# Kernel optimization log

Hardware: AMD Instinct MI355X
Metric: run time of the kernel (lower is better)

## Reference

```python
import jax, jax.numpy as jnp
import numpy as np

N_NODES = 100000
D = 256
B = 64
EPG = 1024           # edges per query group in the last (pruned) layer
E1 = B * EPG         # 65536
E0 = 65536
K = 256              # max_edges


def setup_inputs() -> dict:
    key = jax.random.key(0)
    ks = jax.random.split(key, 20)
    # last-layer edges: sorted by eg_idx, exactly EPG edges per query group
    eg_idx1 = np.repeat(np.arange(B, dtype=np.int32), EPG)
    node_i1 = np.asarray(jax.random.randint(ks[0], (E1,), 0, N_NODES, dtype=jnp.int32))
    node_j1 = np.asarray(jax.random.randint(ks[1], (E1,), 0, N_NODES, dtype=jnp.int32))
    edges1 = np.zeros((E1, 8), dtype=np.int32)
    edges1[:, 0] = eg_idx1; edges1[:, 6] = node_i1; edges1[:, 7] = node_j1
    # earlier-layer edges (no pruning, any order)
    edges0 = np.zeros((E0, 8), dtype=np.int32)
    edges0[:, 0] = np.asarray(jax.random.randint(ks[2], (E0,), 0, B, dtype=jnp.int32))
    edges0[:, 6] = np.asarray(jax.random.randint(ks[3], (E0,), 0, N_NODES, dtype=jnp.int32))
    edges0[:, 7] = np.asarray(jax.random.randint(ks[4], (E0,), 0, N_NODES, dtype=jnp.int32))

    rn = lambda k, s, sc=1.0: (jax.random.normal(k, s, dtype=jnp.float32) * sc)
    return {
        "attended_nodes": jax.random.randint(ks[5], (B, 2), 0, N_NODES, dtype=jnp.int32),
        "node_score": jax.random.uniform(ks[6], (N_NODES,), dtype=jnp.float32),
        "edges0": jnp.asarray(edges0),
        "edges1": jnp.asarray(edges1),
        "rel_emb0": rn(ks[7], (E0, D)),
        "rel_emb1": rn(ks[8], (E1, D)),
        "memorized_embedding": rn(ks[9], (N_NODES, D)),
        "query_src_ts_emb": rn(ks[10], (B, D)),
        "query_rel_emb": rn(ks[11], (B, D)),
        "Wl": rn(ks[12], (4 * D, 2 * D), np.sqrt(2.0 / (4 * D))),
        "bl": rn(ks[13], (2 * D,), 0.01),
        "Wr": rn(ks[14], (4 * D, 2 * D), np.sqrt(2.0 / (4 * D))),
        "br": rn(ks[15], (2 * D,), 0.01),
        "Wc": rn(ks[16], (2 * D, 2 * D), np.sqrt(2.0 / (4 * D))),
        "bc": rn(ks[17], (2 * D,), 0.01),
        "Wlin": rn(ks[18], (D, D), np.sqrt(2.0 / D)),
        "blin": rn(ks[19], (D,), 0.01),
        "max_edges": K,
    }


def _g_score(hi, hj, rel, qs, qr, Wl, bl, Wr, br, Wc, bc):
    # bilinear MLP score: sum(LReLU(L @ Wl) * ((LReLU(R @ Wr)) @ Wc), -1)
    left = jnp.concatenate([hi, rel, qs, qr], axis=-1)   # [E, 4D]
    right = jnp.concatenate([hj, rel, qs, qr], axis=-1)  # [E, 4D]
    l = jax.nn.leaky_relu(left @ Wl + bl)                # [E, 2D]
    r = jax.nn.leaky_relu(right @ Wr + br) @ Wc + bc     # [E, 2D]
    return jnp.sum(l * r, axis=-1)                       # [E]


def _att_score(edges, emb, rel, qs_tab, qr_tab, Wl, bl, Wr, br, Wc, bc):
    hi = emb[edges[:, 6]]
    hj = emb[edges[:, 7]]
    qs = qs_tab[edges[:, 0]]
    qr = qr_tab[edges[:, 0]]
    return _g_score(hi, hj, rel, qs, qr, Wl, bl, Wr, br, Wc, bc)


def _segment_softmax(logits, seg, num_seg):
    m = jax.ops.segment_max(logits, seg, num_segments=num_seg)
    e = jnp.exp(logits - m[seg])
    s = jax.ops.segment_sum(e, seg, num_segments=num_seg)
    return e / s[seg]


def _update_nodes(edges, emb, logits):
    # aggregate source embeddings into targets, weighted by attention;
    # nodes with no incoming edge keep their old embedding.
    n = emb.shape[0]
    agg = jax.ops.segment_sum(logits[:, None] * emb[edges[:, 6]], edges[:, 7], num_segments=n)
    cnt = jax.ops.segment_sum(jnp.ones_like(logits), edges[:, 7], num_segments=n)
    return jnp.where((cnt > 0)[:, None], agg, emb)


def reference(attended_nodes, node_score, edges0, edges1, rel_emb0, rel_emb1,
              memorized_embedding, query_src_ts_emb, query_rel_emb,
              Wl, bl, Wr, br, Wc, bc, Wlin, blin, max_edges):
    n_nodes = memorized_embedding.shape[0]
    # ---- last layer: attention + segmented softmax over source node ----
    logits1 = _att_score(edges1, memorized_embedding, rel_emb1,
                         query_src_ts_emb, query_rel_emb, Wl, bl, Wr, br, Wc, bc)
    sm1 = _segment_softmax(logits1, edges1[:, 6], n_nodes)
    src_att = node_score[edges1[:, 6]]
    target_att = sm1 * src_att
    # ---- per-query top-k pruning (groups are contiguous, equal size EPG) ----
    b = B
    vals = target_att.reshape(b, EPG)
    pruned_att2, idx = jax.lax.top_k(vals, max_edges)              # [B, K]
    orig_indices = (jnp.arange(b, dtype=idx.dtype)[:, None] * EPG + idx).reshape(-1)
    pruned_att = pruned_att2.reshape(-1)                           # [B*K]
    pruned_edges = edges1[orig_indices]
    sm_pruned = sm1[orig_indices]
    # ---- node score aggregation ('sum') ----
    updated_node_score = jax.ops.segment_sum(sm_pruned * pruned_att,
                                             pruned_edges[:, 7], num_segments=n_nodes)
    # ---- propagate representations along pruned edges ----
    emb = _update_nodes(pruned_edges, memorized_embedding, sm_pruned)
    # ---- earlier layers (reversed) ----
    logits0 = _att_score(edges0, emb, rel_emb0, query_src_ts_emb, query_rel_emb,
                         Wl, bl, Wr, br, Wc, bc)
    sm0 = _segment_softmax(logits0, edges0[:, 6], n_nodes)
    emb = _update_nodes(edges0, emb, sm0)
    # ---- bypass: linear + LeakyReLU between steps ----
    emb = jax.nn.leaky_relu(emb @ Wlin + blin)
    return updated_node_score, emb, pruned_edges, orig_indices
```

## Files before the change

### kernel.cpp

```cpp
#include <hip/hip_runtime.h>
#include <math.h>


#define NNODES 100000
#define DDIM   256
#define NH     512
#define NGROUP 64
#define EPG    1024
#define E1N    65536
#define E0N    65536
#define KTOP   256

typedef __attribute__((ext_vector_type(8))) _Float16 h8v;
typedef __attribute__((ext_vector_type(4))) float f32x4;
typedef __attribute__((ext_vector_type(4))) int i4v;

__device__ __forceinline__ float lrelu(float x) { return x > 0.0f ? x : 0.01f * x; }

__device__ __forceinline__ unsigned fenc(float f) {
  unsigned u = __float_as_uint(f);
  return (u & 0x80000000u) ? ~u : (u | 0x80000000u);
}
__device__ __forceinline__ float fdec(unsigned k) {
  unsigned u = (k & 0x80000000u) ? (k & 0x7FFFFFFFu) : ~k;
  return __uint_as_float(u);
}

__device__ __forceinline__ void splitf(float v, unsigned short& h, unsigned short& l) {
  _Float16 hh = (_Float16)v;
  _Float16 ll = (_Float16)(v - (float)hh);
  h = __builtin_bit_cast(unsigned short, hh);
  l = __builtin_bit_cast(unsigned short, ll);
}

__device__ __forceinline__ unsigned packsplit(float v) {
  unsigned short h, l;
  splitf(v, h, l);
  return ((unsigned)h << 16) | (unsigned)l;
}

__device__ __forceinline__ f32x4 mfma16(h8v a, h8v b, f32x4 c) {
  return __builtin_amdgcn_mfma_f32_16x16x32_f16(a, b, c, 0, 0, 0);
}

__global__ __launch_bounds__(512)
void qterm_kernel(const float* __restrict__ qse, const float* __restrict__ qre,
                  const float* __restrict__ Wl, const float* __restrict__ bl,
                  const float* __restrict__ Wr, const float* __restrict__ br,
                  float* __restrict__ qtl, float* __restrict__ qtr)
{
  const int g = blockIdx.x;
  const int o = threadIdx.x;
  __shared__ float sq[DDIM];
  __shared__ float sr[DDIM];
  if (o < DDIM) sq[o] = qse[(size_t)g * DDIM + o];
  else          sr[o - DDIM] = qre[(size_t)g * DDIM + (o - DDIM)];
  __syncthreads();
  float al = bl[o], ar = br[o];
  for (int k = 0; k < DDIM; ++k) {
    float a = sq[k], b = sr[k];
    al += a * Wl[(size_t)(512 + k) * NH + o] + b * Wl[(size_t)(768 + k) * NH + o];
    ar += a * Wr[(size_t)(512 + k) * NH + o] + b * Wr[(size_t)(768 + k) * NH + o];
  }
  qtl[(size_t)g * NH + o] = al;
  qtr[(size_t)g * NH + o] = ar;
}

__global__ __launch_bounds__(256)
void wprep_kernel(const float* __restrict__ Wl, const float* __restrict__ Wr,
                  const float* __restrict__ Wc,
                  unsigned short* __restrict__ WltH, unsigned short* __restrict__ WltL,
                  unsigned short* __restrict__ WrtH, unsigned short* __restrict__ WrtL,
                  unsigned short* __restrict__ WctH, unsigned short* __restrict__ WctL)
{
  __shared__ float shv[32][33];
  const int mtx = blockIdx.y;
  const int ti = blockIdx.x >> 4;
  const int tj = blockIdx.x & 15;
  const float* W = mtx == 0 ? Wl : (mtx == 1 ? Wr : Wc);
  unsigned short* OH = mtx == 0 ? WltH : (mtx == 1 ? WrtH : WctH);
  unsigned short* OL = mtx == 0 ? WltL : (mtx == 1 ? WrtL : WctL);
  const int t = threadIdx.x;
  const int r = t >> 3, c4 = (t & 7) * 4;
  *(float4*)&shv[r][c4] = *(const float4*)(W + (size_t)(ti * 32 + r) * 512 + tj * 32 + c4);
  __syncthreads();
  unsigned short h[4], l[4];
#pragma unroll
  for (int q = 0; q < 4; ++q) splitf(shv[c4 + q][r], h[q], l[q]);
  const size_t off = (size_t)(tj * 32 + r) * 512 + ti * 32 + c4;
  *(uint2*)(OH + off) = make_uint2((unsigned)h[0] | ((unsigned)h[1] << 16),
                                   (unsigned)h[2] | ((unsigned)h[3] << 16));
  *(uint2*)(OL + off) = make_uint2((unsigned)l[0] | ((unsigned)l[1] << 16),
                                   (unsigned)l[2] | ((unsigned)l[3] << 16));
}

__global__ __launch_bounds__(256)
void wlinprep_kernel(const float* __restrict__ Wlin, unsigned short* __restrict__ WlinT)
{
  __shared__ float shv[32][33];
  const int ti = blockIdx.x >> 3;
  const int tj = blockIdx.x & 7;
  const int t = threadIdx.x;
  const int r = t >> 3, c4 = (t & 7) * 4;
  *(float4*)&shv[r][c4] = *(const float4*)(Wlin + (size_t)(ti * 32 + r) * 256 + tj * 32 + c4);
  __syncthreads();
  unsigned short o[4];
#pragma unroll
  for (int q = 0; q < 4; ++q)
    o[q] = __builtin_bit_cast(unsigned short, (_Float16)shv[c4 + q][r]);
  *(uint2*)(WlinT + (size_t)(tj * 32 + r) * 256 + ti * 32 + c4) =
      make_uint2((unsigned)o[0] | ((unsigned)o[1] << 16),
                 (unsigned)o[2] | ((unsigned)o[3] << 16));
}

template<int SPLIT>
__global__ __launch_bounds__(512, 2)
void fused_score_kernel(const int* __restrict__ edges,
                        const float* __restrict__ emb,
                        const float* __restrict__ rel,
                        const unsigned short* __restrict__ BrH,
                        const unsigned short* __restrict__ BrL,
                        const unsigned short* __restrict__ BcH,
                        const unsigned short* __restrict__ BcL,
                        const unsigned short* __restrict__ BlH,
                        const unsigned short* __restrict__ BlL,
                        const float* __restrict__ qtr,
                        const float* __restrict__ qtl,
                        const float* __restrict__ bcv,
                        float* __restrict__ logits,
                        unsigned* __restrict__ mkey)
{
  __shared__ unsigned lds[64 * 512];
  __shared__ float red[8][64];
  __shared__ int sidx[64];
  __shared__ int sgrp[64];

  const int tid  = threadIdx.x;
  const int lane = tid & 63;
  const int w    = tid >> 6;
  const int arow = lane & 15;
  const int kgrp = (lane >> 4) * 8;
  const int col0 = w * 64;
  const int rb   = blockIdx.x * 64;

  auto stage = [&]() {
    const int srow = tid >> 3;
    const int sseg = tid & 7;
    const float* src = (sseg < 4)
        ? emb + (size_t)sidx[srow] * DDIM + sseg * 64
        : rel + (size_t)(rb + srow) * DDIM + (sseg - 4) * 64;
    const int sw = (srow & 7) << 2;
#pragma unroll
    for (int q = 0; q < 16; ++q) {
      float4 f = ((const float4*)src)[q];
      uint4 o = make_uint4(packsplit(f.x), packsplit(f.y), packsplit(f.z), packsplit(f.w));
      *(uint4*)&lds[srow * 512 + ((sseg * 64 + q * 4) ^ sw)] = o;
    }
  };

  auto gemm = [&](const unsigned short* BH, const unsigned short* BL, f32x4 (&acc)[4][4]) {
    for (int ks = 0; ks < 16; ++ks) {
      const int k0 = ks * 32 + kgrp;
      h8v bh[4], bl[4];
#pragma unroll
      for (int nt = 0; nt < 4; ++nt) {
        const size_t boff = (size_t)(col0 + nt * 16 + arow) * 512 + k0;
        bh[nt] = *(const h8v*)(BH + boff);
        if (SPLIT) bl[nt] = *(const h8v*)(BL + boff);
      }
#pragma unroll
      for (int mt = 0; mt < 4; ++mt) {
        const int row = mt * 16 + arow;
        const int sw = (row & 7) << 2;
        const unsigned* lp = &lds[row * 512];
        uint4 u0 = *(const uint4*)(lp + (k0 ^ sw));
        uint4 u1 = *(const uint4*)(lp + ((k0 + 4) ^ sw));
        unsigned u[8] = {u0.x, u0.y, u0.z, u0.w, u1.x, u1.y, u1.z, u1.w};
        i4v hv, lv;
#pragma unroll
        for (int d = 0; d < 4; ++d) {
          hv[d] = (int)((u[2*d] >> 16) | (u[2*d+1] & 0xffff0000u));
          if (SPLIT) lv[d] = (int)((u[2*d] & 0xffffu) | (u[2*d+1] << 16));
        }
        h8v h = __builtin_bit_cast(h8v, hv);
        h8v l;
        if (SPLIT) l = __builtin_bit_cast(h8v, lv);
#pragma unroll
        for (int nt = 0; nt < 4; ++nt) {
          acc[mt][nt] = mfma16(h, bh[nt], acc[mt][nt]);
          if (SPLIT) {
            acc[mt][nt] = mfma16(h, bl[nt], acc[mt][nt]);
            acc[mt][nt] = mfma16(l, bh[nt], acc[mt][nt]);
          }
        }
      }
    }
  };

  if (tid < 64) {
    const int* er = edges + (size_t)(rb + tid) * 8;
    sidx[tid] = er[7];
    sgrp[tid] = er[0];
  }
  __syncthreads();
  stage();
  __syncthreads();

  f32x4 a1[4][4];
#pragma unroll
  for (int a = 0; a < 4; ++a)
#pragma unroll
    for (int b = 0; b < 4; ++b) a1[a][b] = (f32x4)0.0f;
  gemm(BrH, BrL, a1);
  __syncthreads();
#pragma unroll
  for (int mt = 0; mt < 4; ++mt)
#pragma unroll
    for (int nt = 0; nt < 4; ++nt) {
      const int c = col0 + nt * 16 + arow;
#pragma unroll
      for (int reg = 0; reg < 4; ++reg) {
        const int row = mt * 16 + (lane >> 4) * 4 + reg;
        float v = lrelu(a1[mt][nt][reg] + qtr[(size_t)sgrp[row] * NH + c]);
        lds[row * 512 + (c ^ ((row & 7) << 2))] = packsplit(v);
      }
    }
  __syncthreads();

  f32x4 ro[4][4];
#pragma unroll
  for (int a = 0; a < 4; ++a)
#pragma unroll
    for (int b = 0; b < 4; ++b) ro[a][b] = (f32x4)0.0f;
  gemm(BcH, BcL, ro);
#pragma unroll
  for (int nt = 0; nt < 4; ++nt) {
    const float bcval = bcv[col0 + nt * 16 + arow];
#pragma unroll
    for (int mt = 0; mt < 4; ++mt)
#pragma unroll
      for (int reg = 0; reg < 4; ++reg) ro[mt][nt][reg] += bcval;
  }
  __syncthreads();
  if (tid < 64) sidx[tid] = edges[(size_t)(rb + tid) * 8 + 6];
  __syncthreads();
  stage();
  __syncthreads();

  f32x4 a3[4][4];
#pragma unroll
  for (int a = 0; a < 4; ++a)
#pragma unroll
    for (int b = 0; b < 4; ++b) a3[a][b] = (f32x4)0.0f;
  gemm(BlH, BlL, a3);
#pragma unroll
  for (int mt = 0; mt < 4; ++mt) {
#pragma unroll
    for (int reg = 0; reg < 4; ++reg) {
      const int row = mt * 16 + (lane >> 4) * 4 + reg;
      const int g = sgrp[row];
      float s = 0.0f;
#pragma unroll
      for (int nt = 0; nt < 4; ++nt) {
        const int c = col0 + nt * 16 + arow;
        float v = lrelu(a3[mt][nt][reg] + qtl[(size_t)g * NH + c]);
        s += v * ro[mt][nt][reg];
      }
      s += __shfl_xor(s, 1); s += __shfl_xor(s, 2);
      s += __shfl_xor(s, 4); s += __shfl_xor(s, 8);
      if ((lane & 15) == 0) red[w][row] = s;
    }
  }
  __syncthreads();
  if (tid < 64) {
    float s = 0.0f;
#pragma unroll
    for (int p = 0; p < 8; ++p) s += red[p][tid];
    logits[rb + tid] = s;
    atomicMax(mkey + sidx[tid], fenc(s));
  }
}

__global__ void smax_exp_kernel(const int* __restrict__ edges, const float* __restrict__ logits,
                                const unsigned* __restrict__ mkey, float* __restrict__ ssum,
                                float* __restrict__ sm, int* __restrict__ cnt, int E)
{
  int e = blockIdx.x * blockDim.x + threadIdx.x;
  if (e < E) {
    int s = edges[(size_t)e * 8 + 6];
    float ev = expf(logits[e] - fdec(mkey[s]));
    sm[e] = ev;
    atomicAdd(ssum + s, ev);
    if (cnt) atomicAdd(cnt + edges[(size_t)e * 8 + 7], 1);
  }
}

__global__ void smax_norm_kernel(const int* __restrict__ edges, const float* __restrict__ ssum,
                                 float* __restrict__ sm, const float* __restrict__ nscore,
                                 float* __restrict__ ta, int E)
{
  int e = blockIdx.x * blockDim.x + threadIdx.x;
  if (e < E) {
    int s = edges[(size_t)e * 8 + 6];
    float v = sm[e] / ssum[s];
    sm[e] = v;
    if (ta) ta[e] = v * nscore[s];
  }
}

__global__ __launch_bounds__(256)
void topk_kernel(const float* __restrict__ ta, const float* __restrict__ sm1,
                 const int* __restrict__ edges1,
                 float* __restrict__ out0, float* __restrict__ out2,
                 float* __restrict__ out3, float* __restrict__ smp,
                 int* __restrict__ prn_i, int* __restrict__ prn_j,
                 int* __restrict__ cnt1)
{
  __shared__ float v[EPG];
  __shared__ int   ix[EPG];
  const int g = blockIdx.x, tid = threadIdx.x;
  for (int t = tid; t < EPG; t += 256) { v[t] = ta[(size_t)g * EPG + t]; ix[t] = t; }
  __syncthreads();
  for (int k = 2; k <= EPG; k <<= 1) {
    for (int j = k >> 1; j > 0; j >>= 1) {
      for (int t = tid; t < EPG; t += 256) {
        int l = t ^ j;
        if (l > t) {
          float va = v[t], vb = v[l];
          int ia = ix[t], ib = ix[l];
          bool aFirst = (va > vb) || (va == vb && ia < ib);
          bool up = ((t & k) == 0);
          bool sw = up ? !aFirst : aFirst;
          if (sw) { v[t] = vb; ix[t] = ib; v[l] = va; ix[l] = ia; }
        }
      }
      __syncthreads();
    }
  }
  const int r = tid;
  const int oi = ix[r];
  const float val = v[r];
  const int orig = g * EPG + oi;
  out3[(size_t)g * KTOP + r] = (float)orig;
  const int* er = edges1 + (size_t)orig * 8;
#pragma unroll
  for (int c = 0; c < 8; ++c)
    out2[((size_t)(g * KTOP + r)) * 8 + c] = (float)er[c];
  const int ii = er[6], jj = er[7];
  const float smv = sm1[orig];
  smp[(size_t)g * KTOP + r] = smv;
  prn_i[(size_t)g * KTOP + r] = ii;
  prn_j[(size_t)g * KTOP + r] = jj;
  atomicAdd(out0 + jj, smv * val);
  atomicAdd(cnt1 + jj, 1);
}

__global__ void scatter_kernel(const int* __restrict__ idx_i, int si,
                               const int* __restrict__ idx_j, int sj,
                               const float* __restrict__ w,
                               const float* __restrict__ semb,
                               float* __restrict__ agg)
{
  const int e0 = blockIdx.x * 4;
  const int o = threadIdx.x;
#pragma unroll
  for (int q = 0; q < 4; ++q) {
    const int e = e0 + q;
    const int i = idx_i[(size_t)e * si];
    const int j = idx_j[(size_t)e * sj];
    atomicAdd(agg + (size_t)j * DDIM + o, w[e] * semb[(size_t)i * DDIM + o]);
  }
}

__global__ void combine_kernel(const float* __restrict__ mememb, const int* __restrict__ cnt,
                               float* __restrict__ agg)
{
  size_t id = (size_t)blockIdx.x * 256 + threadIdx.x;
  if (cnt[id >> 8] == 0) agg[id] = mememb[id];
}

__global__ __launch_bounds__(512)
void final_mfma_kernel(const float* __restrict__ emb1, const float* __restrict__ agg0,
                       const int* __restrict__ cnt0,
                       const unsigned short* __restrict__ WlinT,
                       const float* __restrict__ blin, float* __restrict__ out)
{
  __shared__ int scnt[128];
  const int tid  = threadIdx.x;
  const int lane = tid & 63;
  const int wid  = tid >> 6;
  const int wm = wid >> 2, wn = wid & 3;
  const int rb = blockIdx.x * 128;
  const int arow = lane & 15;
  const int kgrp = (lane >> 4) * 8;
  const int row0 = wm * 64;
  const int col0 = wn * 64;

  if (tid < 128) {
    int r = rb + tid;
    scnt[tid] = (r < NNODES) ? cnt0[(r < NNODES) ? r : 0] : 0;
  }
  __syncthreads();

  f32x4 acc[4][4];
#pragma unroll
  for (int a = 0; a < 4; ++a)
#pragma unroll
    for (int b = 0; b < 4; ++b) acc[a][b] = (f32x4)0.0f;

  for (int ks = 0; ks < 8; ++ks) {
    const int k0 = ks * 32 + kgrp;
    h8v ah[4], bh[4];
#pragma unroll
    for (int nt = 0; nt < 4; ++nt)
      bh[nt] = *(const h8v*)(WlinT + (size_t)(col0 + nt * 16 + arow) * 256 + k0);
#pragma unroll
    for (int mt = 0; mt < 4; ++mt) {
      const int rl = row0 + mt * 16 + arow;
      int r = rb + rl;
      int rc = (r < NNODES) ? r : (NNODES - 1);
      const float* base = (scnt[rl] > 0) ? agg0 : emb1;
      const float* src = base + (size_t)rc * DDIM + k0;
      float4 f0 = *(const float4*)src;
      float4 f1 = *(const float4*)(src + 4);
      float v[8] = {f0.x, f0.y, f0.z, f0.w, f1.x, f1.y, f1.z, f1.w};
      h8v h;
#pragma unroll
      for (int d = 0; d < 8; ++d) h[d] = (_Float16)v[d];
      ah[mt] = h;
    }
#pragma unroll
    for (int mt = 0; mt < 4; ++mt)
#pragma unroll
      for (int nt = 0; nt < 4; ++nt)
        acc[mt][nt] = mfma16(ah[mt], bh[nt], acc[mt][nt]);
  }

  float bl4[4];
#pragma unroll
  for (int nt = 0; nt < 4; ++nt) bl4[nt] = blin[col0 + nt * 16 + arow];

#pragma unroll
  for (int mt = 0; mt < 4; ++mt)
#pragma unroll
    for (int reg = 0; reg < 4; ++reg) {
      const int r = rb + row0 + mt * 16 + (lane >> 4) * 4 + reg;
      if (r < NNODES) {
#pragma unroll
        for (int nt = 0; nt < 4; ++nt) {
          const int c = col0 + nt * 16 + arow;
          out[(size_t)r * DDIM + c] = lrelu(acc[mt][nt][reg] + bl4[nt]);
        }
      }
    }
}

extern "C" void kernel_launch(void* const* d_in, const int* in_sizes, int n_in,
                              void* d_out, int out_size, void* d_ws, size_t ws_size,
                              hipStream_t stream)
{
  (void)in_sizes; (void)n_in; (void)out_size; (void)ws_size;

  const float* node_score = (const float*)d_in[1];
  const int*   edges0 = (const int*)d_in[2];
  const int*   edges1 = (const int*)d_in[3];
  const float* rel0   = (const float*)d_in[4];
  const float* rel1   = (const float*)d_in[5];
  const float* mememb = (const float*)d_in[6];
  const float* qse    = (const float*)d_in[7];
  const float* qre    = (const float*)d_in[8];
  const float* Wl     = (const float*)d_in[9];
  const float* bl     = (const float*)d_in[10];
  const float* Wr     = (const float*)d_in[11];
  const float* br     = (const float*)d_in[12];
  const float* Wc     = (const float*)d_in[13];
  const float* bc     = (const float*)d_in[14];
  const float* Wlin   = (const float*)d_in[15];
  const float* blin   = (const float*)d_in[16];

  float* out0 = (float*)d_out;
  float* out1 = out0 + NNODES;
  float* out2 = out1 + (size_t)NNODES * DDIM;
  float* out3 = out2 + (size_t)NGROUP * KTOP * 8;

  char* wptr = (char*)d_ws;
  auto alloc = [&](size_t bytes) -> char* {
    char* p = wptr;
    wptr += (bytes + 255) & ~(size_t)255;
    return p;
  };
  float*    qtl     = (float*)alloc((size_t)NGROUP * NH * 4);
  float*    qtr     = (float*)alloc((size_t)NGROUP * NH * 4);
  float*    logits1 = (float*)alloc((size_t)E1N * 4);
  float*    sm1     = (float*)alloc((size_t)E1N * 4);
  float*    ta      = (float*)alloc((size_t)E1N * 4);
  float*    logits0 = (float*)alloc((size_t)E0N * 4);
  float*    sm0     = (float*)alloc((size_t)E0N * 4);
  unsigned* mkey    = (unsigned*)alloc((size_t)NNODES * 4);
  float*    ssum    = (float*)alloc((size_t)NNODES * 4);
  int*      cnt1    = (int*)alloc((size_t)NNODES * 4);
  int*      cnt0    = (int*)alloc((size_t)NNODES * 4);
  float*    smp     = (float*)alloc((size_t)NGROUP * KTOP * 4);
  int*      prn_i   = (int*)alloc((size_t)NGROUP * KTOP * 4);
  int*      prn_j   = (int*)alloc((size_t)NGROUP * KTOP * 4);
  float*    agg1    = (float*)alloc((size_t)NNODES * DDIM * 4);

  unsigned short* WltH = (unsigned short*)alloc((size_t)512 * 512 * 2);
  unsigned short* WltL = (unsigned short*)alloc((size_t)512 * 512 * 2);
  unsigned short* WrtH = (unsigned short*)alloc((size_t)512 * 512 * 2);
  unsigned short* WrtL = (unsigned short*)alloc((size_t)512 * 512 * 2);
  unsigned short* WctH = (unsigned short*)alloc((size_t)512 * 512 * 2);
  unsigned short* WctL = (unsigned short*)alloc((size_t)512 * 512 * 2);
  unsigned short* WlnT = (unsigned short*)alloc((size_t)256 * 256 * 2);

  (void)hipMemsetAsync(agg1, 0, (size_t)NNODES * DDIM * 4, stream);
  (void)hipMemsetAsync(cnt1, 0, (size_t)NNODES * 4, stream);
  (void)hipMemsetAsync(mkey, 0, (size_t)NNODES * 4, stream);
  (void)hipMemsetAsync(ssum, 0, (size_t)NNODES * 4, stream);
  (void)hipMemsetAsync(out0, 0, (size_t)NNODES * 4, stream);

  qterm_kernel<<<NGROUP, 512, 0, stream>>>(qse, qre, Wl, bl, Wr, br, qtl, qtr);
  {
    dim3 g(256, 3);
    wprep_kernel<<<g, 256, 0, stream>>>(Wl, Wr, Wc, WltH, WltL, WrtH, WrtL, WctH, WctL);
  }
  wlinprep_kernel<<<64, 256, 0, stream>>>(Wlin, WlnT);

  fused_score_kernel<1><<<E1N / 64, 512, 0, stream>>>(
      edges1, mememb, rel1, WrtH, WrtL, WctH, WctL, WltH, WltL,
      qtr, qtl, bc, logits1, mkey);

  smax_exp_kernel<<<E1N / 256, 256, 0, stream>>>(edges1, logits1, mkey, ssum, sm1,
                                                 nullptr, E1N);
  smax_norm_kernel<<<E1N / 256, 256, 0, stream>>>(edges1, ssum, sm1, node_score, ta, E1N);
  topk_kernel<<<NGROUP, 256, 0, stream>>>(ta, sm1, edges1, out0, out2, out3,
                                          smp, prn_i, prn_j, cnt1);
  scatter_kernel<<<NGROUP * KTOP / 4, 256, 0, stream>>>(prn_i, 1, prn_j, 1, smp,
                                                        mememb, agg1);
  combine_kernel<<<NNODES, 256, 0, stream>>>(mememb, cnt1, agg1);

  (void)hipMemsetAsync(mkey, 0, (size_t)NNODES * 4, stream);
  (void)hipMemsetAsync(ssum, 0, (size_t)NNODES * 4, stream);
  (void)hipMemsetAsync(cnt0, 0, (size_t)NNODES * 4, stream);
  (void)hipMemsetAsync(out1, 0, (size_t)NNODES * DDIM * 4, stream);

  fused_score_kernel<0><<<E0N / 64, 512, 0, stream>>>(
      edges0, agg1, rel0, WrtH, WrtL, WctH, WctL, WltH, WltL,
      qtr, qtl, bc, logits0, mkey);

  smax_exp_kernel<<<E0N / 256, 256, 0, stream>>>(edges0, logits0, mkey, ssum, sm0,
                                                 cnt0, E0N);
  smax_norm_kernel<<<E0N / 256, 256, 0, stream>>>(edges0, ssum, sm0, nullptr, nullptr, E0N);
  scatter_kernel<<<E0N / 4, 256, 0, stream>>>(edges0 + 6, 8, edges0 + 7, 8, sm0,
                                              agg1, out1);
  final_mfma_kernel<<<(NNODES + 127) / 128, 512, 0, stream>>>(agg1, out1, cnt0,
                                                              WlnT, blin, out1);
}
```

Measured before the change: 1.102 ms.

## Split LDS into separate hi/lo fp16 planes and prefetch second-stage rows into registers

The fused score kernel now stores the split-fp16 operands as two separate planes (hi and lo) with an XOR swizzle at 8-element granularity. This lets the GEMM inner loop read h8v fragments straight from LDS instead of unpacking interleaved 32-bit words with shifts and masks. The emb[node_i] and rel rows used by the third GEMM are loaded into 16 uint4 registers at kernel start, so their global latency overlaps the first two GEMMs. The cost is much higher register pressure under launch_bounds(512,2), which risks spills, and the second LReLU writeback now does scattered 16-bit LDS stores.

```diff
diff --git a/kernel.cpp b/kernel.cpp
--- a/kernel.cpp
+++ b/kernel.cpp
@@ -13,7 +13,6 @@
 
 typedef __attribute__((ext_vector_type(8))) _Float16 h8v;
 typedef __attribute__((ext_vector_type(4))) float f32x4;
-typedef __attribute__((ext_vector_type(4))) int i4v;
 
 __device__ __forceinline__ float lrelu(float x) { return x > 0.0f ? x : 0.01f * x; }
 
@@ -33,14 +32,26 @@
   l = __builtin_bit_cast(unsigned short, ll);
 }
 
-__device__ __forceinline__ unsigned packsplit(float v) {
-  unsigned short h, l;
-  splitf(v, h, l);
-  return ((unsigned)h << 16) | (unsigned)l;
-}
-
 __device__ __forceinline__ f32x4 mfma16(h8v a, h8v b, f32x4 c) {
   return __builtin_amdgcn_mfma_f32_16x16x32_f16(a, b, c, 0, 0, 0);
+}
+
+__device__ __forceinline__ void pack8(uint4 a, uint4 b, uint4& ph, uint4& pl) {
+  float v[8] = {__uint_as_float(a.x), __uint_as_float(a.y),
+                __uint_as_float(a.z), __uint_as_float(a.w),
+                __uint_as_float(b.x), __uint_as_float(b.y),
+                __uint_as_float(b.z), __uint_as_float(b.w)};
+  unsigned short h[8], l[8];
+#pragma unroll
+  for (int d = 0; d < 8; ++d) splitf(v[d], h[d], l[d]);
+  ph = make_uint4((unsigned)h[0] | ((unsigned)h[1] << 16),
+                  (unsigned)h[2] | ((unsigned)h[3] << 16),
+                  (unsigned)h[4] | ((unsigned)h[5] << 16),
+                  (unsigned)h[6] | ((unsigned)h[7] << 16));
+  pl = make_uint4((unsigned)l[0] | ((unsigned)l[1] << 16),
+                  (unsigned)l[2] | ((unsigned)l[3] << 16),
+                  (unsigned)l[4] | ((unsigned)l[5] << 16),
+                  (unsigned)l[6] | ((unsigned)l[7] << 16));
 }
 
 __global__ __launch_bounds__(512)
@@ -130,37 +141,68 @@
                         float* __restrict__ logits,
                         unsigned* __restrict__ mkey)
 {
-  __shared__ unsigned lds[64 * 512];
+  constexpr int NP = SPLIT ? 2 : 1;
+  __shared__ uint4 planesv[NP * 4096];
   __shared__ float red[8][64];
-  __shared__ int sidx[64];
-  __shared__ int sgrp[64];
+  __shared__ int sidxJ[64], sidxI[64], sgrp[64];
 
   const int tid  = threadIdx.x;
   const int lane = tid & 63;
   const int w    = tid >> 6;
   const int arow = lane & 15;
-  const int kgrp = (lane >> 4) * 8;
+  const int grp  = lane >> 4;
   const int col0 = w * 64;
   const int rb   = blockIdx.x * 64;
 
-  auto stage = [&]() {
-    const int srow = tid >> 3;
-    const int sseg = tid & 7;
-    const float* src = (sseg < 4)
-        ? emb + (size_t)sidx[srow] * DDIM + sseg * 64
-        : rel + (size_t)(rb + srow) * DDIM + (sseg - 4) * 64;
-    const int sw = (srow & 7) << 2;
-#pragma unroll
-    for (int q = 0; q < 16; ++q) {
-      float4 f = ((const float4*)src)[q];
-      uint4 o = make_uint4(packsplit(f.x), packsplit(f.y), packsplit(f.z), packsplit(f.w));
-      *(uint4*)&lds[srow * 512 + ((sseg * 64 + q * 4) ^ sw)] = o;
-    }
-  };
-
-  auto gemm = [&](const unsigned short* BH, const unsigned short* BL, f32x4 (&acc)[4][4]) {
+  const int srow = tid >> 3;
+  const int gs   = tid & 7;
+  const int ssw  = srow & 7;
+
+  if (tid < 64) {
+    const int* er = edges + (size_t)(rb + tid) * 8;
+    sgrp[tid]  = er[0];
+    sidxI[tid] = er[6];
+    sidxJ[tid] = er[7];
+  }
+  __syncthreads();
+
+  const float* baseR = rel + (size_t)(rb + srow) * DDIM - 256;
+
+  uint4 ai[16];
+  {
+    const float* bI = emb + (size_t)sidxI[srow] * DDIM;
+#pragma unroll
+    for (int q = 0; q < 8; ++q) {
+      const int kf = q * 64 + ((gs ^ ssw) << 3);
+      const float* s = (q < 4) ? (bI + kf) : (baseR + kf);
+      ai[2 * q]     = ((const uint4*)s)[0];
+      ai[2 * q + 1] = ((const uint4*)s)[1];
+    }
+  }
+
+  {
+    const float* bJ = emb + (size_t)sidxJ[srow] * DDIM;
+#pragma unroll
+    for (int q = 0; q < 8; ++q) {
+      const int kf = q * 64 + ((gs ^ ssw) << 3);
+      const float* s = (q < 4) ? (bJ + kf) : (baseR + kf);
+      uint4 f0 = ((const uint4*)s)[0];
+      uint4 f1 = ((const uint4*)s)[1];
+      uint4 ph, pl;
+      pack8(f0, f1, ph, pl);
+      planesv[srow * 64 + q * 8 + gs] = ph;
+      if (SPLIT) planesv[4096 + srow * 64 + q * 8 + gs] = pl;
+    }
+  }
+  __syncthreads();
+
+  const unsigned short* hiP = (const unsigned short*)planesv;
+  const unsigned short* loP = hiP + 4096 * 8;
+
+  auto gemm = [&](const unsigned short* BH, const unsigned short* BL,
+                  f32x4 (&acc)[4][4]) {
     for (int ks = 0; ks < 16; ++ks) {
-      const int k0 = ks * 32 + kgrp;
+      const int k0 = ks * 32 + grp * 8;
       h8v bh[4], bl[4];
 #pragma unroll
       for (int nt = 0; nt < 4; ++nt) {
@@ -171,20 +213,10 @@
 #pragma unroll
       for (int mt = 0; mt < 4; ++mt) {
         const int row = mt * 16 + arow;
-        const int sw = (row & 7) << 2;
-        const unsigned* lp = &lds[row * 512];
-        uint4 u0 = *(const uint4*)(lp + (k0 ^ sw));
-        uint4 u1 = *(const uint4*)(lp + ((k0 + 4) ^ sw));
-        unsigned u[8] = {u0.x, u0.y, u0.z, u0.w, u1.x, u1.y, u1.z, u1.w};
-        i4v hv, lv;
-#pragma unroll
-        for (int d = 0; d < 4; ++d) {
-          hv[d] = (int)((u[2*d] >> 16) | (u[2*d+1] & 0xffff0000u));
-          if (SPLIT) lv[d] = (int)((u[2*d] & 0xffffu) | (u[2*d+1] << 16));
-        }
-        h8v h = __builtin_bit_cast(h8v, hv);
+        const int gh = (ks * 4 + grp) ^ (row & 7);
+        h8v h = *(const h8v*)(hiP + row * 512 + gh * 8);
         h8v l;
-        if (SPLIT) l = __builtin_bit_cast(h8v, lv);
+        if (SPLIT) l = *(const h8v*)(loP + row * 512 + gh * 8);
 #pragma unroll
         for (int nt = 0; nt < 4; ++nt) {
           acc[mt][nt] = mfma16(h, bh[nt], acc[mt][nt]);
@@ -197,15 +229,6 @@
     }
   };
 
-  if (tid < 64) {
-    const int* er = edges + (size_t)(rb + tid) * 8;
-    sidx[tid] = er[7];
-    sgrp[tid] = er[0];
-  }
-  __syncthreads();
-  stage();
-  __syncthreads();
-
   f32x4 a1[4][4];
 #pragma unroll
   for (int a = 0; a < 4; ++a)
@@ -213,18 +236,27 @@
     for (int b = 0; b < 4; ++b) a1[a][b] = (f32x4)0.0f;
   gemm(BrH, BrL, a1);
   __syncthreads();
-#pragma unroll
-  for (int mt = 0; mt < 4; ++mt)
-#pragma unroll
-    for (int nt = 0; nt < 4; ++nt) {
-      const int c = col0 + nt * 16 + arow;
-#pragma unroll
-      for (int reg = 0; reg < 4; ++reg) {
-        const int row = mt * 16 + (lane >> 4) * 4 + reg;
-        float v = lrelu(a1[mt][nt][reg] + qtr[(size_t)sgrp[row] * NH + c]);
-        lds[row * 512 + (c ^ ((row & 7) << 2))] = packsplit(v);
+
+  {
+    unsigned short* hiW = (unsigned short*)planesv;
+    unsigned short* loW = hiW + 4096 * 8;
+#pragma unroll
+    for (int mt = 0; mt < 4; ++mt)
+#pragma unroll
+      for (int nt = 0; nt < 4; ++nt) {
+        const int c = col0 + nt * 16 + arow;
+#pragma unroll
+        for (int reg = 0; reg < 4; ++reg) {
+          const int row = mt * 16 + grp * 4 + reg;
+          float v = lrelu(a1[mt][nt][reg] + qtr[(size_t)sgrp[row] * NH + c]);
+          unsigned short h, l;
+          splitf(v, h, l);
+          const int off = row * 512 + (((c >> 3) ^ (row & 7)) << 3) + (c & 7);
+          hiW[off] = h;
+          if (SPLIT) loW[off] = l;
+        }
       }
-    }
+  }
   __syncthreads();
 
   f32x4 ro[4][4];
@@ -242,9 +274,14 @@
       for (int reg = 0; reg < 4; ++reg) ro[mt][nt][reg] += bcval;
   }
   __syncthreads();
-  if (tid < 64) sidx[tid] = edges[(size_t)(rb + tid) * 8 + 6];
-  __syncthreads();
-  stage();
+
+#pragma unroll
+  for (int q = 0; q < 8; ++q) {
+    uint4 ph, pl;
+    pack8(ai[2 * q], ai[2 * q + 1], ph, pl);
+    planesv[srow * 64 + q * 8 + gs] = ph;
+    if (SPLIT) planesv[4096 + srow * 64 + q * 8 + gs] = pl;
+  }
   __syncthreads();
 
   f32x4 a3[4][4];
@@ -257,7 +294,7 @@
   for (int mt = 0; mt < 4; ++mt) {
 #pragma unroll
     for (int reg = 0; reg < 4; ++reg) {
-      const int row = mt * 16 + (lane >> 4) * 4 + reg;
+      const int row = mt * 16 + grp * 4 + reg;
       const int g = sgrp[row];
       float s = 0.0f;
 #pragma unroll
@@ -277,7 +314,7 @@
 #pragma unroll
     for (int p = 0; p < 8; ++p) s += red[p][tid];
     logits[rb + tid] = s;
-    atomicMax(mkey + sidx[tid], fenc(s));
+    atomicMax(mkey + sidxI[tid], fenc(s));
   }
 }
 
```

New measurement: 1.051 ms. 1.05x faster.
